# Performance work log

Measured on AMD Instinct MI355X. Metric: run time of the kernel, lower is better.

## Reference

```python
import jax, jax.numpy as jnp
import numpy as np

N_NODES = 100000
N_PAIRS = 1600000
F = 64
H = 4
D = F // H  # head dim = 16


def setup_inputs() -> dict:
    key = jax.random.key(0)
    ks = jax.random.split(key, 9)
    x = jax.random.normal(ks[0], (N_NODES, F), dtype=jnp.float32)
    w_ij = jax.random.normal(ks[1], (N_PAIRS, F), dtype=jnp.float32)
    phi_r_cut = jax.random.uniform(ks[2], (N_PAIRS,), dtype=jnp.float32)
    pair_mask = jnp.ones((N_PAIRS,), dtype=jnp.float32)
    Wq = jax.random.normal(ks[3], (H, D, D), dtype=jnp.float32) / np.sqrt(D)
    Wk = jax.random.normal(ks[4], (H, D, D), dtype=jnp.float32) / np.sqrt(D)
    Wv = jax.random.normal(ks[5], (H, D, D), dtype=jnp.float32) / np.sqrt(D)
    idx_i = jnp.sort(jax.random.randint(ks[6], (N_PAIRS,), 0, N_NODES)).astype(jnp.int64)
    idx_j = jax.random.randint(ks[7], (N_PAIRS,), 0, N_NODES).astype(jnp.int64)
    return {"x": x, "w_ij": w_ij, "phi_r_cut": phi_r_cut, "pair_mask": pair_mask,
            "Wq": Wq, "Wk": Wk, "Wv": Wv, "idx_i": idx_i, "idx_j": idx_j}


def reference(x, w_ij, phi_r_cut, pair_mask, Wq, Wk, Wv, idx_i, idx_j):
    n, f = x.shape
    h, d, _ = Wq.shape
    xh = x.reshape(n, h, d)            # (n, H, D) head split
    wh = w_ij.reshape(-1, h, d)        # (p, H, D)
    # per-head projections (Dense with no bias: x @ kernel), then gather by edge
    q_i = jnp.einsum('nhd,hde->nhe', xh, Wq)[idx_i]   # (p, H, D)
    k_j = jnp.einsum('nhd,hde->nhe', xh, Wk)[idx_j]   # (p, H, D)
    alpha = (q_i * wh * k_j).sum(axis=-1) / jnp.sqrt(jnp.asarray(d, x.dtype))  # (p, H)
    alpha = alpha * (pair_mask * phi_r_cut)[:, None]  # safe_scale with cutoff * mask
    v_j = jnp.einsum('nhd,hde->nhe', xh, Wv)[idx_j]   # (p, H, D)
    out = jax.ops.segment_sum(alpha[..., None] * v_j, idx_i, num_segments=n)  # (n, H, D)
    return out.reshape(n, f)
```

## Files before the change

### kernel.cpp

```cpp
#include <hip/hip_runtime.h>
#include <stdint.h>

#define N_NODES_C 100000
#define N_PAIRS_C 1600000
#define FDIM 64
#define HH 4
#define DD 16

__global__ __launch_bounds__(256) void qkv_kernel(
    const float* __restrict__ x,
    const float* __restrict__ Wq,
    const float* __restrict__ Wk,
    const float* __restrict__ Wv,
    float* __restrict__ q,
    float* __restrict__ k,
    float* __restrict__ v)
{
    __shared__ float sWq[HH][DD * DD + 8];
    __shared__ float sWk[HH][DD * DD + 8];
    __shared__ float sWv[HH][DD * DD + 8];
    for (int t = threadIdx.x; t < HH * DD * DD; t += 256) {
        sWq[t >> 8][t & 255] = Wq[t];
        sWk[t >> 8][t & 255] = Wk[t];
        sWv[t >> 8][t & 255] = Wv[t];
    }
    __syncthreads();

    int gid = blockIdx.x * 256 + threadIdx.x;
    int n = gid >> 2;
    int h = gid & 3;
    if (n >= N_NODES_C) return;

    const float* xp = x + (int64_t)n * FDIM + h * DD;
    float xr[DD];
#pragma unroll
    for (int d0 = 0; d0 < DD; d0 += 4) {
        float4 t4 = *reinterpret_cast<const float4*>(xp + d0);
        xr[d0 + 0] = t4.x; xr[d0 + 1] = t4.y; xr[d0 + 2] = t4.z; xr[d0 + 3] = t4.w;
    }

    float qo[DD], ko[DD], vo[DD];
#pragma unroll
    for (int e = 0; e < DD; e++) { qo[e] = 0.f; ko[e] = 0.f; vo[e] = 0.f; }

    const float* wqh = sWq[h];
    const float* wkh = sWk[h];
    const float* wvh = sWv[h];
#pragma unroll
    for (int d = 0; d < DD; d++) {
        float xv = xr[d];
#pragma unroll
        for (int e = 0; e < DD; e++) {
            qo[e] = fmaf(xv, wqh[d * DD + e], qo[e]);
            ko[e] = fmaf(xv, wkh[d * DD + e], ko[e]);
            vo[e] = fmaf(xv, wvh[d * DD + e], vo[e]);
        }
    }

    int64_t base = (int64_t)n * FDIM + h * DD;
#pragma unroll
    for (int e0 = 0; e0 < DD; e0 += 4) {
        *reinterpret_cast<float4*>(q + base + e0) = make_float4(qo[e0], qo[e0+1], qo[e0+2], qo[e0+3]);
        *reinterpret_cast<float4*>(k + base + e0) = make_float4(ko[e0], ko[e0+1], ko[e0+2], ko[e0+3]);
        *reinterpret_cast<float4*>(v + base + e0) = make_float4(vo[e0], vo[e0+1], vo[e0+2], vo[e0+3]);
    }
}

__global__ __launch_bounds__(256) void pair_kernel(
    const float* __restrict__ q,
    const float* __restrict__ k,
    const float* __restrict__ v,
    const float* __restrict__ w_ij,
    const float* __restrict__ phi,
    const float* __restrict__ mask,
    const int*  __restrict__ idx_i,
    const int*  __restrict__ idx_j,
    float* __restrict__ out,
    int pairs_per_group)
{
    int gid = blockIdx.x * 256 + threadIdx.x;
    int grp = gid >> 4;
    int m   = threadIdx.x & 15;

    int64_t start = (int64_t)grp * pairs_per_group;
    if (start >= N_PAIRS_C) return;
    int64_t end = start + pairs_per_group;
    if (end > N_PAIRS_C) end = N_PAIRS_C;

    const float4* w4p = reinterpret_cast<const float4*>(w_ij);
    const float4* q4p = reinterpret_cast<const float4*>(q);
    const float4* k4p = reinterpret_cast<const float4*>(k);
    const float4* v4p = reinterpret_cast<const float4*>(v);

    int64_t p1 = (start + 1 < end) ? start + 1 : end - 1;
    int   i_a = idx_i[start];
    int   j_a = idx_j[start];
    float s_a = phi[start] * mask[start];
    int   i_b = idx_i[p1];
    int   j_b = idx_j[p1];
    float s_b = phi[p1] * mask[p1];

    float4 w_a = w4p[start * DD + m];
    float4 k_a = k4p[(int64_t)j_a * DD + m];
    float4 v_a = v4p[(int64_t)j_a * DD + m];

    float4 q4  = q4p[(int64_t)i_a * DD + m];
    int cur_i  = i_a;
    float4 acc = make_float4(0.f, 0.f, 0.f, 0.f);

    for (int64_t p = start; p < end; ++p) {
        int64_t p2 = (p + 2 < end) ? p + 2 : end - 1;
        int   i_c = idx_i[p2];
        int   j_c = idx_j[p2];
        float s_c = phi[p2] * mask[p2];

        int64_t pn = (p + 1 < end) ? p + 1 : end - 1;
        float4 w_b = w4p[pn * DD + m];
        float4 k_b = k4p[(int64_t)j_b * DD + m];
        float4 v_b = v4p[(int64_t)j_b * DD + m];

        if (i_a != cur_i) {
            int64_t ob = (int64_t)cur_i * FDIM + m * 4;
            atomicAdd(&out[ob + 0], acc.x);
            atomicAdd(&out[ob + 1], acc.y);
            atomicAdd(&out[ob + 2], acc.z);
            atomicAdd(&out[ob + 3], acc.w);
            acc = make_float4(0.f, 0.f, 0.f, 0.f);
            q4 = q4p[(int64_t)i_a * DD + m];
            cur_i = i_a;
        }

        float r = q4.x * w_a.x * k_a.x
                + q4.y * w_a.y * k_a.y
                + q4.z * w_a.z * k_a.z
                + q4.w * w_a.w * k_a.w;
        r += __shfl_xor(r, 1);
        r += __shfl_xor(r, 2);
        float alpha = r * 0.25f * s_a;

        acc.x = fmaf(alpha, v_a.x, acc.x);
        acc.y = fmaf(alpha, v_a.y, acc.y);
        acc.z = fmaf(alpha, v_a.z, acc.z);
        acc.w = fmaf(alpha, v_a.w, acc.w);

        i_a = i_b; j_a = j_b; s_a = s_b;
        w_a = w_b; k_a = k_b; v_a = v_b;
        i_b = i_c; j_b = j_c; s_b = s_c;
    }

    {
        int64_t ob = (int64_t)cur_i * FDIM + m * 4;
        atomicAdd(&out[ob + 0], acc.x);
        atomicAdd(&out[ob + 1], acc.y);
        atomicAdd(&out[ob + 2], acc.z);
        atomicAdd(&out[ob + 3], acc.w);
    }
}

extern "C" void kernel_launch(void* const* d_in, const int* in_sizes, int n_in,
                              void* d_out, int out_size, void* d_ws, size_t ws_size,
                              hipStream_t stream) {
    const float* x       = (const float*)d_in[0];
    const float* w_ij    = (const float*)d_in[1];
    const float* phi     = (const float*)d_in[2];
    const float* mask    = (const float*)d_in[3];
    const float* Wq      = (const float*)d_in[4];
    const float* Wk      = (const float*)d_in[5];
    const float* Wv      = (const float*)d_in[6];
    const int*   idx_i   = (const int*)d_in[7];
    const int*   idx_j   = (const int*)d_in[8];
    float* out = (float*)d_out;

    float* q = (float*)d_ws;
    float* k = q + (int64_t)N_NODES_C * FDIM;
    float* v = k + (int64_t)N_NODES_C * FDIM;

    hipMemsetAsync(d_out, 0, (size_t)out_size * sizeof(float), stream);

    int qkv_blocks = (N_NODES_C * HH + 255) / 256;
    qkv_kernel<<<qkv_blocks, 256, 0, stream>>>(x, Wq, Wk, Wv, q, k, v);

    const int n_groups = 32768;
    int pairs_per_group = (N_PAIRS_C + n_groups - 1) / n_groups;
    pair_kernel<<<n_groups / 16, 256, 0, stream>>>(q, k, v, w_ij, phi, mask,
                                                   idx_i, idx_j, out, pairs_per_group);
}
```

Baseline: 723.0 us.

## Store K and V interleaved in fp16 and stream w_ij with nontemporal loads

The QKV projection now writes K and V as a single interleaved half-precision array, so each pair gathers one 16-byte load per lane instead of two 16-byte fp32 loads. This halves the random-gather traffic for K/V in the pair loop. The w_ij stream is read with nontemporal loads so it does not evict the gathered K/V lines from cache. The cost is fp16 rounding of K and V, which may affect accuracy.

```diff
diff --git a/kernel.cpp b/kernel.cpp
--- a/kernel.cpp
+++ b/kernel.cpp
@@ -1,4 +1,5 @@
 #include <hip/hip_runtime.h>
+#include <hip/hip_fp16.h>
 #include <stdint.h>
 
 #define N_NODES_C 100000
@@ -7,14 +8,15 @@
 #define HH 4
 #define DD 16
 
+typedef float vf4 __attribute__((ext_vector_type(4)));
+
 __global__ __launch_bounds__(256) void qkv_kernel(
     const float* __restrict__ x,
     const float* __restrict__ Wq,
     const float* __restrict__ Wk,
     const float* __restrict__ Wv,
     float* __restrict__ q,
-    float* __restrict__ k,
-    float* __restrict__ v)
+    __half* __restrict__ kv)
 {
     __shared__ float sWq[HH][DD * DD + 8];
     __shared__ float sWk[HH][DD * DD + 8];
@@ -57,19 +59,24 @@
         }
     }
 
-    int64_t base = (int64_t)n * FDIM + h * DD;
+    int64_t qbase = (int64_t)n * FDIM + h * DD;
 #pragma unroll
     for (int e0 = 0; e0 < DD; e0 += 4) {
-        *reinterpret_cast<float4*>(q + base + e0) = make_float4(qo[e0], qo[e0+1], qo[e0+2], qo[e0+3]);
-        *reinterpret_cast<float4*>(k + base + e0) = make_float4(ko[e0], ko[e0+1], ko[e0+2], ko[e0+3]);
-        *reinterpret_cast<float4*>(v + base + e0) = make_float4(vo[e0], vo[e0+1], vo[e0+2], vo[e0+3]);
+        *reinterpret_cast<float4*>(q + qbase + e0) = make_float4(qo[e0], qo[e0+1], qo[e0+2], qo[e0+3]);
     }
+
+    __half2 kvh[DD];
+#pragma unroll
+    for (int e = 0; e < DD; e++) kvh[e] = __floats2half2_rn(ko[e], vo[e]);
+    uint4* dst = reinterpret_cast<uint4*>(kv + (int64_t)n * 128 + h * 32);
+    const uint4* src = reinterpret_cast<const uint4*>(kvh);
+#pragma unroll
+    for (int t = 0; t < 4; t++) dst[t] = src[t];
 }
 
 __global__ __launch_bounds__(256) void pair_kernel(
     const float* __restrict__ q,
-    const float* __restrict__ k,
-    const float* __restrict__ v,
+    const __half* __restrict__ kv,
     const float* __restrict__ w_ij,
     const float* __restrict__ phi,
     const float* __restrict__ mask,
@@ -87,10 +94,8 @@
     int64_t end = start + pairs_per_group;
     if (end > N_PAIRS_C) end = N_PAIRS_C;
 
-    const float4* w4p = reinterpret_cast<const float4*>(w_ij);
+    const vf4*   w4p = reinterpret_cast<const vf4*>(w_ij);
     const float4* q4p = reinterpret_cast<const float4*>(q);
-    const float4* k4p = reinterpret_cast<const float4*>(k);
-    const float4* v4p = reinterpret_cast<const float4*>(v);
 
     int64_t p1 = (start + 1 < end) ? start + 1 : end - 1;
     int   i_a = idx_i[start];
@@ -100,9 +105,8 @@
     int   j_b = idx_j[p1];
     float s_b = phi[p1] * mask[p1];
 
-    float4 w_a = w4p[start * DD + m];
-    float4 k_a = k4p[(int64_t)j_a * DD + m];
-    float4 v_a = v4p[(int64_t)j_a * DD + m];
+    vf4   w_a  = __builtin_nontemporal_load(w4p + start * DD + m);
+    uint4 kv_a = *reinterpret_cast<const uint4*>(kv + (int64_t)j_a * 128 + m * 8);
 
     float4 q4  = q4p[(int64_t)i_a * DD + m];
     int cur_i  = i_a;
@@ -115,9 +119,8 @@
         float s_c = phi[p2] * mask[p2];
 
         int64_t pn = (p + 1 < end) ? p + 1 : end - 1;
-        float4 w_b = w4p[pn * DD + m];
-        float4 k_b = k4p[(int64_t)j_b * DD + m];
-        float4 v_b = v4p[(int64_t)j_b * DD + m];
+        vf4   w_b  = __builtin_nontemporal_load(w4p + pn * DD + m);
+        uint4 kv_b = *reinterpret_cast<const uint4*>(kv + (int64_t)j_b * 128 + m * 8);
 
         if (i_a != cur_i) {
             int64_t ob = (int64_t)cur_i * FDIM + m * 4;
@@ -130,21 +133,27 @@
             cur_i = i_a;
         }
 
-        float r = q4.x * w_a.x * k_a.x
-                + q4.y * w_a.y * k_a.y
-                + q4.z * w_a.z * k_a.z
-                + q4.w * w_a.w * k_a.w;
+        const __half2* hp = reinterpret_cast<const __half2*>(&kv_a);
+        float2 e0 = __half22float2(hp[0]);
+        float2 e1 = __half22float2(hp[1]);
+        float2 e2 = __half22float2(hp[2]);
+        float2 e3 = __half22float2(hp[3]);
+
+        float r = q4.x * w_a.x * e0.x
+                + q4.y * w_a.y * e1.x
+                + q4.z * w_a.z * e2.x
+                + q4.w * w_a.w * e3.x;
         r += __shfl_xor(r, 1);
         r += __shfl_xor(r, 2);
         float alpha = r * 0.25f * s_a;
 
-        acc.x = fmaf(alpha, v_a.x, acc.x);
-        acc.y = fmaf(alpha, v_a.y, acc.y);
-        acc.z = fmaf(alpha, v_a.z, acc.z);
-        acc.w = fmaf(alpha, v_a.w, acc.w);
+        acc.x = fmaf(alpha, e0.y, acc.x);
+        acc.y = fmaf(alpha, e1.y, acc.y);
+        acc.z = fmaf(alpha, e2.y, acc.z);
+        acc.w = fmaf(alpha, e3.y, acc.w);
 
         i_a = i_b; j_a = j_b; s_a = s_b;
-        w_a = w_b; k_a = k_b; v_a = v_b;
+        w_a = w_b; kv_a = kv_b;
         i_b = i_c; j_b = j_c; s_b = s_c;
     }
 
@@ -171,17 +180,16 @@
     const int*   idx_j   = (const int*)d_in[8];
     float* out = (float*)d_out;
 
-    float* q = (float*)d_ws;
-    float* k = q + (int64_t)N_NODES_C * FDIM;
-    float* v = k + (int64_t)N_NODES_C * FDIM;
+    float*  q  = (float*)d_ws;
+    __half* kv = (__half*)(q + (int64_t)N_NODES_C * FDIM);
 
     hipMemsetAsync(d_out, 0, (size_t)out_size * sizeof(float), stream);
 
     int qkv_blocks = (N_NODES_C * HH + 255) / 256;
-    qkv_kernel<<<qkv_blocks, 256, 0, stream>>>(x, Wq, Wk, Wv, q, k, v);
+    qkv_kernel<<<qkv_blocks, 256, 0, stream>>>(x, Wq, Wk, Wv, q, kv);
 
     const int n_groups = 32768;
     int pairs_per_group = (N_PAIRS_C + n_groups - 1) / n_groups;
-    pair_kernel<<<n_groups / 16, 256, 0, stream>>>(q, k, v, w_ij, phi, mask,
+    pair_kernel<<<n_groups / 16, 256, 0, stream>>>(q, kv, w_ij, phi, mask,
                                                    idx_i, idx_j, out, pairs_per_group);
 }
```

Result: faster. 674.6 us (-6.7%).
